# Performance work log

Measured on AMD Instinct MI355X. Metric: run time of the kernel, lower is better.

The kernel has to match this reference:

```python
import jax, jax.numpy as jnp
import numpy as np

N = 50000      # nodes
E = 800000     # edges in normalized A (incl. self loops)
DIN = 128      # input_dim
DOUT = 64      # output_dim
BN_EPS = 1e-5
SLOPE = 0.01   # LeakyReLU default negative slope


def setup_inputs() -> dict:
    key = jax.random.key(0)
    ks = jax.random.split(key, 10)
    H = jax.random.normal(ks[0], (N, DIN), dtype=jnp.float32)
    rows = jax.random.randint(ks[1], (E,), 0, N, dtype=jnp.int32)
    cols = jax.random.randint(ks[2], (E,), 0, N, dtype=jnp.int32)
    # values of the symmetrically normalized adjacency (precomputed in __init__)
    vals = jax.random.uniform(ks[3], (E,), dtype=jnp.float32)
    # BatchNorm1d params/buffers (eval mode: use running stats)
    gamma = 1.0 + 0.1 * jax.random.normal(ks[4], (DIN,), dtype=jnp.float32)
    beta = 0.1 * jax.random.normal(ks[5], (DIN,), dtype=jnp.float32)
    run_mean = 0.1 * jax.random.normal(ks[6], (DIN,), dtype=jnp.float32)
    run_var = 0.5 + jax.random.uniform(ks[7], (DIN,), dtype=jnp.float32)
    # Linear(input_dim, output_dim)
    W = jax.random.normal(ks[8], (DIN, DOUT), dtype=jnp.float32) / np.sqrt(DIN)
    b = 0.01 * jax.random.normal(ks[9], (DOUT,), dtype=jnp.float32)
    return dict(H=H, rows=rows, cols=cols, vals=vals, gamma=gamma, beta=beta,
                run_mean=run_mean, run_var=run_var, W=W, b=b)


def reference(H, rows, cols, vals, gamma, beta, run_mean, run_var, W, b):
    # F.normalize: L2 row normalization with eps=1e-12
    norm = jnp.maximum(jnp.linalg.norm(H, axis=1, keepdims=True), 1e-12)
    Hn = H / norm
    # BatchNorm1d (eval: running stats); dropout is identity in eval
    scale = gamma * jax.lax.rsqrt(run_var + BN_EPS)
    Hb = (Hn - run_mean) * scale + beta
    # Linear projection [N, DIN] @ [DIN, DOUT]
    X = Hb @ W + b
    # SpMM: out[r] = sum_{e: rows[e]==r} vals[e] * X[cols[e]]
    msgs = vals[:, None] * X[cols]            # [E, DOUT] gather + scale
    out = jax.ops.segment_sum(msgs, rows, num_segments=N)
    # LeakyReLU
    return jnp.where(out >= 0, out, SLOPE * out)
```

## Files before the change

kernel.cpp:

```cpp
#include <hip/hip_runtime.h>

#define N_NODES 50000
#define E_EDGES 800000
#define DIN 128
#define DOUT 64
#define NBUK 196
#define CHUNK 4096
#define NBLKA 196
#define ASTRIDE 136

typedef short short8 __attribute__((ext_vector_type(8)));
typedef float f32x4 __attribute__((ext_vector_type(4)));

static __device__ __forceinline__ short f2bf(float f)
{
    union { float f; unsigned u; } x{f};
    const unsigned r = x.u + 0x7FFFu + ((x.u >> 16) & 1u);
    return (short)(r >> 16);
}

__global__ void k_prep(const float* __restrict__ W, const float* __restrict__ gamma,
                       const float* __restrict__ beta, const float* __restrict__ mean,
                       const float* __restrict__ var,
                       unsigned short* __restrict__ Wt, float* __restrict__ sc,
                       float* __restrict__ sh)
{
    const int idx = blockIdx.x * 256 + threadIdx.x;
    const int n = idx >> 7, k = idx & 127;
    Wt[n * DIN + k] = (unsigned short)f2bf(W[k * DOUT + n]);
    if (idx < DIN) {
        const float s = gamma[idx] / sqrtf(var[idx] + 1e-5f);
        sc[idx] = s;
        sh[idx] = beta[idx] - mean[idx] * s;
    }
}

__global__ __launch_bounds__(256) void k_x(
    const float* __restrict__ H, const float* __restrict__ sc,
    const float* __restrict__ sh, const unsigned short* __restrict__ Wt,
    const float* __restrict__ bias, float* __restrict__ X)
{
    __shared__ short A_s[64][ASTRIDE];
    __shared__ short B_s[64][ASTRIDE];
    const int t = threadIdx.x;
    const int l = t & 63, wv = t >> 6;
    const int R0 = blockIdx.x * 64;

    {
        const int rloc = t >> 2, sub = t & 3;
        const int r = R0 + rloc;
        float4 h[8];
        if (r < N_NODES) {
            const float4* hp = (const float4*)(H + (size_t)r * DIN + sub * 32);
#pragma unroll
            for (int i = 0; i < 8; ++i) h[i] = hp[i];
        } else {
#pragma unroll
            for (int i = 0; i < 8; ++i) h[i] = make_float4(0.f, 0.f, 0.f, 0.f);
        }
        float ss = 0.f;
#pragma unroll
        for (int i = 0; i < 8; ++i)
            ss += h[i].x * h[i].x + h[i].y * h[i].y + h[i].z * h[i].z + h[i].w * h[i].w;
        ss += __shfl_xor(ss, 1, 64);
        ss += __shfl_xor(ss, 2, 64);
        const float inv = 1.0f / fmaxf(sqrtf(ss), 1e-12f);

        const float4* scp = (const float4*)(sc + sub * 32);
        const float4* shp = (const float4*)(sh + sub * 32);
#pragma unroll
        for (int i = 0; i < 8; ++i) {
            const float4 s4 = scp[i], b4 = shp[i];
            const float e0 = h[i].x * inv * s4.x + b4.x;
            const float e1 = h[i].y * inv * s4.y + b4.y;
            const float e2 = h[i].z * inv * s4.z + b4.z;
            const float e3 = h[i].w * inv * s4.w + b4.w;
            const unsigned u0 = (unsigned short)f2bf(e0) | ((unsigned)(unsigned short)f2bf(e1) << 16);
            const unsigned u1 = (unsigned short)f2bf(e2) | ((unsigned)(unsigned short)f2bf(e3) << 16);
            *(uint2*)&A_s[rloc][sub * 32 + i * 4] = make_uint2(u0, u1);
        }
    }
    {
        const int n = t >> 2, koff = (t & 3) * 32;
        const uint4* src = (const uint4*)(Wt + n * DIN + koff);
#pragma unroll
        for (int i = 0; i < 4; ++i)
            *(uint4*)&B_s[n][koff + i * 8] = src[i];
    }
    __syncthreads();

    const int ml = l & 15, q = l >> 4;
    f32x4 c0, c1, c2, c3;
    {
        const float b0 = bias[ml],      b1 = bias[16 + ml];
        const float b2 = bias[32 + ml], b3 = bias[48 + ml];
        c0 = f32x4{b0, b0, b0, b0};
        c1 = f32x4{b1, b1, b1, b1};
        c2 = f32x4{b2, b2, b2, b2};
        c3 = f32x4{b3, b3, b3, b3};
    }
#pragma unroll
    for (int k0 = 0; k0 < 4; ++k0) {
        const short8 a  = *(const short8*)&A_s[wv * 16 + ml][k0 * 32 + q * 8];
        const short8 b0 = *(const short8*)&B_s[ml][k0 * 32 + q * 8];
        const short8 b1 = *(const short8*)&B_s[16 + ml][k0 * 32 + q * 8];
        const short8 b2 = *(const short8*)&B_s[32 + ml][k0 * 32 + q * 8];
        const short8 b3 = *(const short8*)&B_s[48 + ml][k0 * 32 + q * 8];
        c0 = __builtin_amdgcn_mfma_f32_16x16x32_bf16(a, b0, c0, 0, 0, 0);
        c1 = __builtin_amdgcn_mfma_f32_16x16x32_bf16(a, b1, c1, 0, 0, 0);
        c2 = __builtin_amdgcn_mfma_f32_16x16x32_bf16(a, b2, c2, 0, 0, 0);
        c3 = __builtin_amdgcn_mfma_f32_16x16x32_bf16(a, b3, c3, 0, 0, 0);
    }
#pragma unroll
    for (int i = 0; i < 4; ++i) {
        const int row = R0 + wv * 16 + q * 4 + i;
        if (row < N_NODES) {
            float* xr = X + (size_t)row * DOUT;
            xr[ml]      = c0[i];
            xr[16 + ml] = c1[i];
            xr[32 + ml] = c2[i];
            xr[48 + ml] = c3[i];
        }
    }
}

__global__ __launch_bounds__(1024) void k_bhist(
    const int* __restrict__ rows, int* __restrict__ hist)
{
    __shared__ int lh[NBUK];
    const int t = threadIdx.x;
    if (t < NBUK) lh[t] = 0;
    __syncthreads();
    const int e0 = blockIdx.x * 8192;
#pragma unroll
    for (int k = 0; k < 8; ++k) {
        const int e = e0 + k * 1024 + t;
        if (e < E_EDGES) atomicAdd(&lh[rows[e] >> 8], 1);
    }
    __syncthreads();
    if (t < NBUK) {
        const int c = lh[t];
        if (c) atomicAdd(&hist[t], c);
    }
}

__global__ __launch_bounds__(256) void k_bscan(
    const int* __restrict__ hist, int* __restrict__ gstart, int* __restrict__ gcursor)
{
    __shared__ int scn[256];
    const int t = threadIdx.x;
    const int v = (t < NBUK) ? hist[t] : 0;
    scn[t] = v;
    __syncthreads();
    for (int o = 1; o < 256; o <<= 1) {
        const int u = (t >= o) ? scn[t - o] : 0;
        __syncthreads();
        scn[t] += u;
        __syncthreads();
    }
    const int ex = scn[t] - v;
    if (t < NBUK) { gstart[t] = ex; gcursor[t] = ex; }
    if (t == NBUK - 1) gstart[NBUK] = ex + v;
}

__global__ __launch_bounds__(256) void k_passA(
    const int* __restrict__ rows, const int* __restrict__ cols,
    const float* __restrict__ vals, int* __restrict__ gcursor,
    uint2* __restrict__ mid)
{
    __shared__ int lhist[NBUK], lstart[NBUK], lcur[NBUK], gbase[NBUK];
    __shared__ int scn[256];
    __shared__ uint2 lbin[CHUNK];
    const int t = threadIdx.x;
    const int e0 = blockIdx.x * CHUNK;
    const int nC = min(CHUNK, E_EDGES - e0);

    if (t < NBUK) lhist[t] = 0;
    __syncthreads();

    uint2 pr[16];
#pragma unroll
    for (int k = 0; k < 16; ++k) {
        const int e = e0 + k * 256 + t;
        if (e < E_EDGES) {
            const int r = rows[e];
            const unsigned pk = (unsigned)cols[e] | ((unsigned)(r & 255) << 16)
                              | ((unsigned)(r >> 8) << 24);
            pr[k] = make_uint2(__float_as_uint(vals[e]), pk);
            atomicAdd(&lhist[r >> 8], 1);
        } else {
            pr[k] = make_uint2(0u, 0xFFFFFFFFu);
        }
    }
    __syncthreads();

    const int v = (t < NBUK) ? lhist[t] : 0;
    scn[t] = v;
    __syncthreads();
    for (int o = 1; o < 256; o <<= 1) {
        const int u = (t >= o) ? scn[t - o] : 0;
        __syncthreads();
        scn[t] += u;
        __syncthreads();
    }
    if (t < NBUK) {
        const int ex = scn[t] - v;
        lstart[t] = ex;
        lcur[t] = ex;
        gbase[t] = v ? atomicAdd(&gcursor[t], v) : 0;
    }
    __syncthreads();

#pragma unroll
    for (int k = 0; k < 16; ++k) {
        const unsigned pk = pr[k].y;
        if (pk != 0xFFFFFFFFu) {
            const int b = pk >> 24;
            const int pos = atomicAdd(&lcur[b], 1);
            lbin[pos] = pr[k];
        }
    }
    __syncthreads();

    for (int i = t; i < nC; i += 256) {
        const uint2 p = lbin[i];
        const int b = p.y >> 24;
        mid[gbase[b] + (i - lstart[b])] = p;
    }
}

__global__ __launch_bounds__(256) void k_passB(
    const int* __restrict__ gstart, const uint2* __restrict__ mid,
    uint2* __restrict__ ev, int* __restrict__ startRow)
{
    __shared__ int lhist[256], scn[256], lcur[256];
    const int t = threadIdx.x;
    const int b = blockIdx.x;
    const int s = gstart[b], e2 = gstart[b + 1];

    lhist[t] = 0;
    __syncthreads();
    for (int i = s + t; i < e2; i += 256)
        atomicAdd(&lhist[(mid[i].y >> 16) & 255], 1);
    __syncthreads();

    const int v = lhist[t];
    scn[t] = v;
    __syncthreads();
    for (int o = 1; o < 256; o <<= 1) {
        const int u = (t >= o) ? scn[t - o] : 0;
        __syncthreads();
        scn[t] += u;
        __syncthreads();
    }
    const int ex = scn[t] - v;
    lcur[t] = ex;
    const int gr = b * 256 + t;
    if (gr <= N_NODES) startRow[gr] = s + ex;
    __syncthreads();

    for (int i = s + t; i < e2; i += 256) {
        const uint2 p = mid[i];
        const int r8 = (p.y >> 16) & 255;
        const int pos = atomicAdd(&lcur[r8], 1);
        ev[s + pos] = make_uint2(p.x, p.y & 0xFFFFu);
    }
}

__global__ __launch_bounds__(256) void k_spmm(
    const int* __restrict__ start, const uint2* __restrict__ ev,
    const float* __restrict__ X, float* __restrict__ out)
{
    const int lane = threadIdx.x & 63;
    const int row  = blockIdx.x * 4 + (threadIdx.x >> 6);
    if (row >= N_NODES) return;
    const int s  = __builtin_amdgcn_readfirstlane(start[row]);
    const int e2 = __builtin_amdgcn_readfirstlane(start[row + 1]);
    float acc = 0.f;
    int c = s;
    for (; c + 3 < e2; c += 4) {
        const uint2 p0 = ev[c],     p1 = ev[c + 1];
        const uint2 p2 = ev[c + 2], p3 = ev[c + 3];
        const float x0 = X[(int)p0.y * DOUT + lane];
        const float x1 = X[(int)p1.y * DOUT + lane];
        const float x2 = X[(int)p2.y * DOUT + lane];
        const float x3 = X[(int)p3.y * DOUT + lane];
        acc = fmaf(__uint_as_float(p0.x), x0, acc);
        acc = fmaf(__uint_as_float(p1.x), x1, acc);
        acc = fmaf(__uint_as_float(p2.x), x2, acc);
        acc = fmaf(__uint_as_float(p3.x), x3, acc);
    }
    for (; c < e2; ++c) {
        const uint2 p = ev[c];
        acc = fmaf(__uint_as_float(p.x), X[(int)p.y * DOUT + lane], acc);
    }
    out[(size_t)row * DOUT + lane] = (acc >= 0.f) ? acc : 0.01f * acc;
}

extern "C" void kernel_launch(void* const* d_in, const int* in_sizes, int n_in,
                              void* d_out, int out_size, void* d_ws, size_t ws_size,
                              hipStream_t stream)
{
    const float* H     = (const float*)d_in[0];
    const int*   rows  = (const int*)  d_in[1];
    const int*   cols  = (const int*)  d_in[2];
    const float* vals  = (const float*)d_in[3];
    const float* gamma = (const float*)d_in[4];
    const float* beta  = (const float*)d_in[5];
    const float* mean  = (const float*)d_in[6];
    const float* var   = (const float*)d_in[7];
    const float* W     = (const float*)d_in[8];
    const float* bias  = (const float*)d_in[9];
    float* out = (float*)d_out;

    char* ws = (char*)d_ws;
    float*          X        = (float*)(ws);
    int*            hist     = (int*)  (ws + 12800000);
    int*            gstart   = (int*)  (ws + 12800800);
    int*            gcursor  = (int*)  (ws + 12801600);
    int*            startRow = (int*)  (ws + 12802400);
    uint2*          mid      = (uint2*)(ws + 13002416);
    uint2*          ev       = (uint2*)(ws + 19402416);
    unsigned short* Wt       = (unsigned short*)(ws + 25802416);
    float*          sc       = (float*)(ws + 25818800);
    float*          sh       = (float*)(ws + 25819312);

    hipMemsetAsync(hist, 0, NBUK * sizeof(int), stream);

    k_prep<<<32, 256, 0, stream>>>(W, gamma, beta, mean, var, Wt, sc, sh);
    k_x<<<(N_NODES + 63) / 64, 256, 0, stream>>>(H, sc, sh, Wt, bias, X);
    k_bhist<<<(E_EDGES + 8191) / 8192, 1024, 0, stream>>>(rows, hist);
    k_bscan<<<1, 256, 0, stream>>>(hist, gstart, gcursor);
    k_passA<<<NBLKA, 256, 0, stream>>>(rows, cols, vals, gcursor, mid);
    k_passB<<<NBUK, 256, 0, stream>>>(gstart, mid, ev, startRow);
    k_spmm<<<(N_NODES + 3) / 4, 256, 0, stream>>>(startRow, ev, X, out);
}
```

Before: 166.9 us.

## Restructure CSR build with fixed-capacity buckets, per-row counts, and half-wave SpMM

Drops the separate bucket-histogram and bucket-scan kernels. Pass A now writes into fixed-capacity bucket regions and counts edges per row with global atomics. A two-level row scan plus an atomic scatter pass replaces the per-bucket sort in pass B, and the SpMM now handles two rows per wave. Each lane loads a float2, and edge metadata is broadcast with shuffles. The intent is fewer launches, more parallel blocks and wider gathers, at the cost of about 800k global atomics, non-deterministic edge order within a row, and a risk of overflow if any bucket exceeds BUKCAP.

```diff
diff --git a/kernel.cpp b/kernel.cpp
--- a/kernel.cpp
+++ b/kernel.cpp
@@ -5,8 +5,7 @@
 #define DIN 128
 #define DOUT 64
 #define NBUK 196
-#define CHUNK 4096
-#define NBLKA 196
+#define BUKCAP 4608
 #define ASTRIDE 136
 
 typedef short short8 __attribute__((ext_vector_type(8)));
@@ -124,32 +123,39 @@
     }
 }
 
-__global__ __launch_bounds__(1024) void k_bhist(
-    const int* __restrict__ rows, int* __restrict__ hist)
-{
-    __shared__ int lh[NBUK];
+__global__ __launch_bounds__(256) void k_passA(
+    const int* __restrict__ rows, const int* __restrict__ cols,
+    const float* __restrict__ vals, int* __restrict__ cnt,
+    int* __restrict__ gcursor, uint2* __restrict__ mid)
+{
+    __shared__ int lhist[NBUK], lstart[NBUK], lcur[NBUK], gbase[NBUK];
+    __shared__ int scn[256];
+    __shared__ uint2 lbin[1024];
     const int t = threadIdx.x;
-    if (t < NBUK) lh[t] = 0;
-    __syncthreads();
-    const int e0 = blockIdx.x * 8192;
-#pragma unroll
-    for (int k = 0; k < 8; ++k) {
-        const int e = e0 + k * 1024 + t;
-        if (e < E_EDGES) atomicAdd(&lh[rows[e] >> 8], 1);
-    }
-    __syncthreads();
-    if (t < NBUK) {
-        const int c = lh[t];
-        if (c) atomicAdd(&hist[t], c);
-    }
-}
-
-__global__ __launch_bounds__(256) void k_bscan(
-    const int* __restrict__ hist, int* __restrict__ gstart, int* __restrict__ gcursor)
-{
-    __shared__ int scn[256];
-    const int t = threadIdx.x;
-    const int v = (t < NBUK) ? hist[t] : 0;
+    const int e0 = blockIdx.x * 1024;
+    const int nC = min(1024, E_EDGES - e0);
+
+    if (t < NBUK) lhist[t] = 0;
+    __syncthreads();
+
+    uint2 pr[4];
+#pragma unroll
+    for (int k = 0; k < 4; ++k) {
+        const int e = e0 + k * 256 + t;
+        if (e < E_EDGES) {
+            const int r = rows[e];
+            pr[k] = make_uint2(__float_as_uint(vals[e]),
+                               (unsigned)cols[e] | ((unsigned)(r & 255) << 16)
+                                                 | ((unsigned)(r >> 8) << 24));
+            atomicAdd(&lhist[r >> 8], 1);
+            atomicAdd(&cnt[r], 1);
+        } else {
+            pr[k] = make_uint2(0u, 0xFFFFFFFFu);
+        }
+    }
+    __syncthreads();
+
+    const int v = (t < NBUK) ? lhist[t] : 0;
     scn[t] = v;
     __syncthreads();
     for (int o = 1; o < 256; o <<= 1) {
@@ -158,143 +164,156 @@
         scn[t] += u;
         __syncthreads();
     }
-    const int ex = scn[t] - v;
-    if (t < NBUK) { gstart[t] = ex; gcursor[t] = ex; }
-    if (t == NBUK - 1) gstart[NBUK] = ex + v;
-}
-
-__global__ __launch_bounds__(256) void k_passA(
-    const int* __restrict__ rows, const int* __restrict__ cols,
-    const float* __restrict__ vals, int* __restrict__ gcursor,
-    uint2* __restrict__ mid)
-{
-    __shared__ int lhist[NBUK], lstart[NBUK], lcur[NBUK], gbase[NBUK];
-    __shared__ int scn[256];
-    __shared__ uint2 lbin[CHUNK];
-    const int t = threadIdx.x;
-    const int e0 = blockIdx.x * CHUNK;
-    const int nC = min(CHUNK, E_EDGES - e0);
-
-    if (t < NBUK) lhist[t] = 0;
-    __syncthreads();
-
-    uint2 pr[16];
-#pragma unroll
-    for (int k = 0; k < 16; ++k) {
-        const int e = e0 + k * 256 + t;
-        if (e < E_EDGES) {
-            const int r = rows[e];
-            const unsigned pk = (unsigned)cols[e] | ((unsigned)(r & 255) << 16)
-                              | ((unsigned)(r >> 8) << 24);
-            pr[k] = make_uint2(__float_as_uint(vals[e]), pk);
-            atomicAdd(&lhist[r >> 8], 1);
-        } else {
-            pr[k] = make_uint2(0u, 0xFFFFFFFFu);
-        }
-    }
-    __syncthreads();
-
-    const int v = (t < NBUK) ? lhist[t] : 0;
-    scn[t] = v;
-    __syncthreads();
-    for (int o = 1; o < 256; o <<= 1) {
-        const int u = (t >= o) ? scn[t - o] : 0;
-        __syncthreads();
-        scn[t] += u;
-        __syncthreads();
-    }
     if (t < NBUK) {
         const int ex = scn[t] - v;
         lstart[t] = ex;
         lcur[t] = ex;
-        gbase[t] = v ? atomicAdd(&gcursor[t], v) : 0;
-    }
-    __syncthreads();
-
-#pragma unroll
-    for (int k = 0; k < 16; ++k) {
+        gbase[t] = t * BUKCAP + (v ? atomicAdd(&gcursor[t], v) : 0);
+    }
+    __syncthreads();
+
+#pragma unroll
+    for (int k = 0; k < 4; ++k) {
         const unsigned pk = pr[k].y;
         if (pk != 0xFFFFFFFFu) {
-            const int b = pk >> 24;
-            const int pos = atomicAdd(&lcur[b], 1);
-            lbin[pos] = pr[k];
+            const int bk = pk >> 24;
+            lbin[atomicAdd(&lcur[bk], 1)] = pr[k];
         }
     }
     __syncthreads();
 
     for (int i = t; i < nC; i += 256) {
         const uint2 p = lbin[i];
-        const int b = p.y >> 24;
-        mid[gbase[b] + (i - lstart[b])] = p;
-    }
-}
-
-__global__ __launch_bounds__(256) void k_passB(
-    const int* __restrict__ gstart, const uint2* __restrict__ mid,
-    uint2* __restrict__ ev, int* __restrict__ startRow)
-{
-    __shared__ int lhist[256], scn[256], lcur[256];
-    const int t = threadIdx.x;
-    const int b = blockIdx.x;
-    const int s = gstart[b], e2 = gstart[b + 1];
-
-    lhist[t] = 0;
-    __syncthreads();
-    for (int i = s + t; i < e2; i += 256)
-        atomicAdd(&lhist[(mid[i].y >> 16) & 255], 1);
-    __syncthreads();
-
-    const int v = lhist[t];
-    scn[t] = v;
-    __syncthreads();
-    for (int o = 1; o < 256; o <<= 1) {
-        const int u = (t >= o) ? scn[t - o] : 0;
-        __syncthreads();
-        scn[t] += u;
-        __syncthreads();
-    }
-    const int ex = scn[t] - v;
-    lcur[t] = ex;
-    const int gr = b * 256 + t;
-    if (gr <= N_NODES) startRow[gr] = s + ex;
-    __syncthreads();
-
-    for (int i = s + t; i < e2; i += 256) {
-        const uint2 p = mid[i];
-        const int r8 = (p.y >> 16) & 255;
-        const int pos = atomicAdd(&lcur[r8], 1);
-        ev[s + pos] = make_uint2(p.x, p.y & 0xFFFFu);
+        const int bk = p.y >> 24;
+        mid[gbase[bk] + (i - lstart[bk])] = p;
+    }
+}
+
+__global__ __launch_bounds__(256) void k_rscan1(
+    const int* __restrict__ cnt, int* __restrict__ startL,
+    int* __restrict__ cursorL, int* __restrict__ bsum)
+{
+    const int b = blockIdx.x, t = threadIdx.x;
+    const int base = b * 1024 + t * 4;
+    int c0 = 0, c1 = 0, c2 = 0, c3 = 0;
+    if (base + 3 < N_NODES) {
+        const int4 c = *(const int4*)(cnt + base);
+        c0 = c.x; c1 = c.y; c2 = c.z; c3 = c.w;
+    } else {
+        if (base     < N_NODES) c0 = cnt[base];
+        if (base + 1 < N_NODES) c1 = cnt[base + 1];
+        if (base + 2 < N_NODES) c2 = cnt[base + 2];
+        if (base + 3 < N_NODES) c3 = cnt[base + 3];
+    }
+    const int s = c0 + c1 + c2 + c3;
+    const int lane = t & 63, wv = t >> 6;
+    int x = s;
+#pragma unroll
+    for (int o = 1; o < 64; o <<= 1) {
+        const int y = __shfl_up(x, o, 64);
+        if (lane >= o) x += y;
+    }
+    __shared__ int wsum[4];
+    if (lane == 63) wsum[wv] = x;
+    __syncthreads();
+    int wpre = 0;
+    for (int i = 0; i < wv; ++i) wpre += wsum[i];
+    const int ex = wpre + x - s;
+    const int p0 = ex, p1 = ex + c0, p2 = p1 + c1, p3 = p2 + c2;
+    if (base + 3 < N_NODES) {
+        *(int4*)(startL + base)  = make_int4(p0, p1, p2, p3);
+        *(int4*)(cursorL + base) = make_int4(p0, p1, p2, p3);
+    } else {
+        const int pv[4] = {p0, p1, p2, p3};
+        for (int i = 0; i < 4; ++i) {
+            if (base + i <= N_NODES) startL[base + i] = pv[i];
+            if (base + i <  N_NODES) cursorL[base + i] = pv[i];
+        }
+    }
+    if (t == 255) bsum[b] = ex + s;
+}
+
+__global__ void k_rscan2(const int* __restrict__ bsum, int* __restrict__ boff)
+{
+    const int lane = threadIdx.x;
+    const int v = (lane < 49) ? bsum[lane] : 0;
+    int x = v;
+#pragma unroll
+    for (int o = 1; o < 64; o <<= 1) {
+        const int y = __shfl_up(x, o, 64);
+        if (lane >= o) x += y;
+    }
+    if (lane < 49) boff[lane] = x - v;
+}
+
+__global__ __launch_bounds__(256) void k_scatter2(
+    const int* __restrict__ gcursor, const uint2* __restrict__ mid,
+    int* __restrict__ cursorL, const int* __restrict__ boff,
+    uint2* __restrict__ ev)
+{
+    const int b  = blockIdx.x / 5;
+    const int sl = blockIdx.x % 5;
+    const int cntb = gcursor[b];
+    const int i0 = sl * 1024;
+    if (i0 >= cntb) return;
+    const int i1 = min(i0 + 1024, cntb);
+    const uint2* src = mid + (size_t)b * BUKCAP;
+    for (int i = i0 + threadIdx.x; i < i1; i += 256) {
+        const uint2 p = src[i];
+        const int row = (b << 8) | ((int)(p.y >> 16) & 255);
+        const int pos = atomicAdd(&cursorL[row], 1) + boff[row >> 10];
+        ev[pos] = make_uint2(p.x, p.y & 0xFFFFu);
     }
 }
 
 __global__ __launch_bounds__(256) void k_spmm(
-    const int* __restrict__ start, const uint2* __restrict__ ev,
-    const float* __restrict__ X, float* __restrict__ out)
+    const int* __restrict__ startL, const int* __restrict__ boff,
+    const uint2* __restrict__ ev, const float* __restrict__ X,
+    float* __restrict__ out)
 {
     const int lane = threadIdx.x & 63;
-    const int row  = blockIdx.x * 4 + (threadIdx.x >> 6);
-    if (row >= N_NODES) return;
-    const int s  = __builtin_amdgcn_readfirstlane(start[row]);
-    const int e2 = __builtin_amdgcn_readfirstlane(start[row + 1]);
-    float acc = 0.f;
-    int c = s;
-    for (; c + 3 < e2; c += 4) {
-        const uint2 p0 = ev[c],     p1 = ev[c + 1];
-        const uint2 p2 = ev[c + 2], p3 = ev[c + 3];
-        const float x0 = X[(int)p0.y * DOUT + lane];
-        const float x1 = X[(int)p1.y * DOUT + lane];
-        const float x2 = X[(int)p2.y * DOUT + lane];
-        const float x3 = X[(int)p3.y * DOUT + lane];
-        acc = fmaf(__uint_as_float(p0.x), x0, acc);
-        acc = fmaf(__uint_as_float(p1.x), x1, acc);
-        acc = fmaf(__uint_as_float(p2.x), x2, acc);
-        acc = fmaf(__uint_as_float(p3.x), x3, acc);
-    }
-    for (; c < e2; ++c) {
-        const uint2 p = ev[c];
-        acc = fmaf(__uint_as_float(p.x), X[(int)p.y * DOUT + lane], acc);
-    }
-    out[(size_t)row * DOUT + lane] = (acc >= 0.f) ? acc : 0.01f * acc;
+    const int hl   = lane & 31;
+    const int sb   = lane & 32;
+    const int row  = blockIdx.x * 8 + ((threadIdx.x >> 6) << 1) + (lane >> 5);
+    const int s  = startL[row] + boff[row >> 10];
+    const int e2 = startL[row + 1] + boff[(row + 1) >> 10];
+    float2 acc = make_float2(0.f, 0.f);
+    for (int c = s; c < e2; c += 32) {
+        const int idx = c + hl;
+        uint2 p = make_uint2(0u, 0u);
+        if (idx < e2) p = ev[idx];
+        const int cnt = min(e2 - c, 32);
+        int j = 0;
+        for (; j + 3 < cnt; j += 4) {
+            const float v0 = __uint_as_float(__shfl((int)p.x, sb + j,     64));
+            const int   c0 = __shfl((int)p.y, sb + j,     64) & 0xFFFF;
+            const float v1 = __uint_as_float(__shfl((int)p.x, sb + j + 1, 64));
+            const int   c1 = __shfl((int)p.y, sb + j + 1, 64) & 0xFFFF;
+            const float v2 = __uint_as_float(__shfl((int)p.x, sb + j + 2, 64));
+            const int   c2 = __shfl((int)p.y, sb + j + 2, 64) & 0xFFFF;
+            const float v3 = __uint_as_float(__shfl((int)p.x, sb + j + 3, 64));
+            const int   c3 = __shfl((int)p.y, sb + j + 3, 64) & 0xFFFF;
+            const float2 x0 = *(const float2*)(X + c0 * DOUT + hl * 2);
+            const float2 x1 = *(const float2*)(X + c1 * DOUT + hl * 2);
+            const float2 x2 = *(const float2*)(X + c2 * DOUT + hl * 2);
+            const float2 x3 = *(const float2*)(X + c3 * DOUT + hl * 2);
+            acc.x = fmaf(v0, x0.x, acc.x); acc.y = fmaf(v0, x0.y, acc.y);
+            acc.x = fmaf(v1, x1.x, acc.x); acc.y = fmaf(v1, x1.y, acc.y);
+            acc.x = fmaf(v2, x2.x, acc.x); acc.y = fmaf(v2, x2.y, acc.y);
+            acc.x = fmaf(v3, x3.x, acc.x); acc.y = fmaf(v3, x3.y, acc.y);
+        }
+        for (; j < cnt; ++j) {
+            const float v = __uint_as_float(__shfl((int)p.x, sb + j, 64));
+            const int  cc = __shfl((int)p.y, sb + j, 64) & 0xFFFF;
+            const float2 xx = *(const float2*)(X + cc * DOUT + hl * 2);
+            acc.x = fmaf(v, xx.x, acc.x);
+            acc.y = fmaf(v, xx.y, acc.y);
+        }
+    }
+    float2 r;
+    r.x = (acc.x >= 0.f) ? acc.x : 0.01f * acc.x;
+    r.y = (acc.y >= 0.f) ? acc.y : 0.01f * acc.y;
+    *(float2*)(out + (size_t)row * DOUT + hl * 2) = r;
 }
 
 extern "C" void kernel_launch(void* const* d_in, const int* in_sizes, int n_in,
@@ -314,24 +333,26 @@
     float* out = (float*)d_out;
 
     char* ws = (char*)d_ws;
-    float*          X        = (float*)(ws);
-    int*            hist     = (int*)  (ws + 12800000);
-    int*            gstart   = (int*)  (ws + 12800800);
-    int*            gcursor  = (int*)  (ws + 12801600);
-    int*            startRow = (int*)  (ws + 12802400);
-    uint2*          mid      = (uint2*)(ws + 13002416);
-    uint2*          ev       = (uint2*)(ws + 19402416);
-    unsigned short* Wt       = (unsigned short*)(ws + 25802416);
-    float*          sc       = (float*)(ws + 25818800);
-    float*          sh       = (float*)(ws + 25819312);
-
-    hipMemsetAsync(hist, 0, NBUK * sizeof(int), stream);
+    float*          X       = (float*)(ws);
+    int*            cnt     = (int*)  (ws + 12800000);
+    int*            gcursor = (int*)  (ws + 13000000);
+    int*            startL  = (int*)  (ws + 13000800);
+    int*            cursorL = (int*)  (ws + 13200816);
+    int*            bsum    = (int*)  (ws + 13400816);
+    int*            boff    = (int*)  (ws + 13401024);
+    uint2*          mid     = (uint2*)(ws + 13401280);
+    uint2*          ev      = (uint2*)(ws + 20626624);
+    unsigned short* Wt      = (unsigned short*)(ws + 27026624);
+    float*          sc      = (float*)(ws + 27043008);
+    float*          sh      = (float*)(ws + 27043520);
+
+    hipMemsetAsync(cnt, 0, 200784, stream);
 
     k_prep<<<32, 256, 0, stream>>>(W, gamma, beta, mean, var, Wt, sc, sh);
     k_x<<<(N_NODES + 63) / 64, 256, 0, stream>>>(H, sc, sh, Wt, bias, X);
-    k_bhist<<<(E_EDGES + 8191) / 8192, 1024, 0, stream>>>(rows, hist);
-    k_bscan<<<1, 256, 0, stream>>>(hist, gstart, gcursor);
-    k_passA<<<NBLKA, 256, 0, stream>>>(rows, cols, vals, gcursor, mid);
-    k_passB<<<NBUK, 256, 0, stream>>>(gstart, mid, ev, startRow);
-    k_spmm<<<(N_NODES + 3) / 4, 256, 0, stream>>>(startRow, ev, X, out);
-}
+    k_passA<<<(E_EDGES + 1023) / 1024, 256, 0, stream>>>(rows, cols, vals, cnt, gcursor, mid);
+    k_rscan1<<<49, 256, 0, stream>>>(cnt, startL, cursorL, bsum);
+    k_rscan2<<<1, 64, 0, stream>>>(bsum, boff);
+    k_scatter2<<<NBUK * 5, 256, 0, stream>>>(gcursor, mid, cursorL, boff, ev);
+    k_spmm<<<N_NODES / 8, 256, 0, stream>>>(startL, boff, ev, X, out);
+}
```

After: 208.1 us. 24.7% more time.

## Replace two-pass CSR build with fixed-capacity row buckets and LDS-atomic SpMM

Applied to the files above, without the earlier changes.

Drops the global bucket histogram, the scan and the second sort pass. Pass A now scatters packed edges straight into fixed-capacity slots per 256-row bucket. The new SpMM gives each bucket one 1024-thread block, which accumulates results with float atomics into 64 KB of LDS and applies LeakyReLU on write-out. This removes kernel launches and a full read/write pass over the edges. The costs are LDS atomic contention, only 196 large blocks, and silent edge loss if any bucket exceeds the fixed capacity, which is only safe for near-uniform row distributions.

```diff
diff --git a/kernel.cpp b/kernel.cpp
--- a/kernel.cpp
+++ b/kernel.cpp
@@ -5,8 +5,9 @@
 #define DIN 128
 #define DOUT 64
 #define NBUK 196
-#define CHUNK 4096
-#define NBLKA 196
+#define BUKCAP 4608
+#define CHUNK 2048
+#define NBLKA 391
 #define ASTRIDE 136
 
 typedef short short8 __attribute__((ext_vector_type(8)));
@@ -124,45 +125,6 @@
     }
 }
 
-__global__ __launch_bounds__(1024) void k_bhist(
-    const int* __restrict__ rows, int* __restrict__ hist)
-{
-    __shared__ int lh[NBUK];
-    const int t = threadIdx.x;
-    if (t < NBUK) lh[t] = 0;
-    __syncthreads();
-    const int e0 = blockIdx.x * 8192;
-#pragma unroll
-    for (int k = 0; k < 8; ++k) {
-        const int e = e0 + k * 1024 + t;
-        if (e < E_EDGES) atomicAdd(&lh[rows[e] >> 8], 1);
-    }
-    __syncthreads();
-    if (t < NBUK) {
-        const int c = lh[t];
-        if (c) atomicAdd(&hist[t], c);
-    }
-}
-
-__global__ __launch_bounds__(256) void k_bscan(
-    const int* __restrict__ hist, int* __restrict__ gstart, int* __restrict__ gcursor)
-{
-    __shared__ int scn[256];
-    const int t = threadIdx.x;
-    const int v = (t < NBUK) ? hist[t] : 0;
-    scn[t] = v;
-    __syncthreads();
-    for (int o = 1; o < 256; o <<= 1) {
-        const int u = (t >= o) ? scn[t - o] : 0;
-        __syncthreads();
-        scn[t] += u;
-        __syncthreads();
-    }
-    const int ex = scn[t] - v;
-    if (t < NBUK) { gstart[t] = ex; gcursor[t] = ex; }
-    if (t == NBUK - 1) gstart[NBUK] = ex + v;
-}
-
 __global__ __launch_bounds__(256) void k_passA(
     const int* __restrict__ rows, const int* __restrict__ cols,
     const float* __restrict__ vals, int* __restrict__ gcursor,
@@ -178,15 +140,15 @@
     if (t < NBUK) lhist[t] = 0;
     __syncthreads();
 
-    uint2 pr[16];
-#pragma unroll
-    for (int k = 0; k < 16; ++k) {
+    uint2 pr[8];
+#pragma unroll
+    for (int k = 0; k < 8; ++k) {
         const int e = e0 + k * 256 + t;
         if (e < E_EDGES) {
             const int r = rows[e];
-            const unsigned pk = (unsigned)cols[e] | ((unsigned)(r & 255) << 16)
-                              | ((unsigned)(r >> 8) << 24);
-            pr[k] = make_uint2(__float_as_uint(vals[e]), pk);
+            pr[k] = make_uint2(__float_as_uint(vals[e]),
+                               (unsigned)cols[e] | ((unsigned)(r & 255) << 16)
+                                                 | ((unsigned)(r >> 8) << 24));
             atomicAdd(&lhist[r >> 8], 1);
         } else {
             pr[k] = make_uint2(0u, 0xFFFFFFFFu);
@@ -207,94 +169,84 @@
         const int ex = scn[t] - v;
         lstart[t] = ex;
         lcur[t] = ex;
-        gbase[t] = v ? atomicAdd(&gcursor[t], v) : 0;
-    }
-    __syncthreads();
-
-#pragma unroll
-    for (int k = 0; k < 16; ++k) {
+        gbase[t] = t * BUKCAP + (v ? atomicAdd(&gcursor[t], v) : 0);
+    }
+    __syncthreads();
+
+#pragma unroll
+    for (int k = 0; k < 8; ++k) {
         const unsigned pk = pr[k].y;
         if (pk != 0xFFFFFFFFu) {
-            const int b = pk >> 24;
-            const int pos = atomicAdd(&lcur[b], 1);
-            lbin[pos] = pr[k];
+            const int bk = pk >> 24;
+            lbin[atomicAdd(&lcur[bk], 1)] = pr[k];
         }
     }
     __syncthreads();
 
     for (int i = t; i < nC; i += 256) {
         const uint2 p = lbin[i];
-        const int b = p.y >> 24;
-        mid[gbase[b] + (i - lstart[b])] = p;
-    }
-}
-
-__global__ __launch_bounds__(256) void k_passB(
-    const int* __restrict__ gstart, const uint2* __restrict__ mid,
-    uint2* __restrict__ ev, int* __restrict__ startRow)
-{
-    __shared__ int lhist[256], scn[256], lcur[256];
+        const int bk = p.y >> 24;
+        const int idx = gbase[bk] + (i - lstart[bk]);
+        if (idx < (bk + 1) * BUKCAP)
+            mid[idx] = p;
+    }
+}
+
+__global__ __launch_bounds__(1024) void k_spmm2(
+    const int* __restrict__ gcursor, const uint2* __restrict__ mid,
+    const float* __restrict__ X, float* __restrict__ out)
+{
+    __shared__ float acc[256 * DOUT];
     const int t = threadIdx.x;
     const int b = blockIdx.x;
-    const int s = gstart[b], e2 = gstart[b + 1];
-
-    lhist[t] = 0;
-    __syncthreads();
-    for (int i = s + t; i < e2; i += 256)
-        atomicAdd(&lhist[(mid[i].y >> 16) & 255], 1);
-    __syncthreads();
-
-    const int v = lhist[t];
-    scn[t] = v;
-    __syncthreads();
-    for (int o = 1; o < 256; o <<= 1) {
-        const int u = (t >= o) ? scn[t - o] : 0;
-        __syncthreads();
-        scn[t] += u;
-        __syncthreads();
-    }
-    const int ex = scn[t] - v;
-    lcur[t] = ex;
-    const int gr = b * 256 + t;
-    if (gr <= N_NODES) startRow[gr] = s + ex;
-    __syncthreads();
-
-    for (int i = s + t; i < e2; i += 256) {
-        const uint2 p = mid[i];
-        const int r8 = (p.y >> 16) & 255;
-        const int pos = atomicAdd(&lcur[r8], 1);
-        ev[s + pos] = make_uint2(p.x, p.y & 0xFFFFu);
-    }
-}
-
-__global__ __launch_bounds__(256) void k_spmm(
-    const int* __restrict__ start, const uint2* __restrict__ ev,
-    const float* __restrict__ X, float* __restrict__ out)
-{
-    const int lane = threadIdx.x & 63;
-    const int row  = blockIdx.x * 4 + (threadIdx.x >> 6);
-    if (row >= N_NODES) return;
-    const int s  = __builtin_amdgcn_readfirstlane(start[row]);
-    const int e2 = __builtin_amdgcn_readfirstlane(start[row + 1]);
-    float acc = 0.f;
-    int c = s;
-    for (; c + 3 < e2; c += 4) {
-        const uint2 p0 = ev[c],     p1 = ev[c + 1];
-        const uint2 p2 = ev[c + 2], p3 = ev[c + 3];
-        const float x0 = X[(int)p0.y * DOUT + lane];
-        const float x1 = X[(int)p1.y * DOUT + lane];
-        const float x2 = X[(int)p2.y * DOUT + lane];
-        const float x3 = X[(int)p3.y * DOUT + lane];
-        acc = fmaf(__uint_as_float(p0.x), x0, acc);
-        acc = fmaf(__uint_as_float(p1.x), x1, acc);
-        acc = fmaf(__uint_as_float(p2.x), x2, acc);
-        acc = fmaf(__uint_as_float(p3.x), x3, acc);
-    }
-    for (; c < e2; ++c) {
-        const uint2 p = ev[c];
-        acc = fmaf(__uint_as_float(p.x), X[(int)p.y * DOUT + lane], acc);
-    }
-    out[(size_t)row * DOUT + lane] = (acc >= 0.f) ? acc : 0.01f * acc;
+    const int lane = t & 63;
+
+    float4* accv = (float4*)acc;
+#pragma unroll
+    for (int k = 0; k < 4; ++k)
+        accv[k * 1024 + t] = make_float4(0.f, 0.f, 0.f, 0.f);
+    __syncthreads();
+
+    const int total = min(__builtin_amdgcn_readfirstlane(gcursor[b]), BUKCAP);
+    const int wv = __builtin_amdgcn_readfirstlane(threadIdx.x >> 6);
+    const int L  = (total + 15) >> 4;
+    const int cs = wv * L;
+    const int ce = min(cs + L, total);
+    const uint2* src = mid + (size_t)b * BUKCAP;
+
+    int c = cs;
+    for (; c + 3 < ce; c += 4) {
+        const uint2 p0 = src[c],     p1 = src[c + 1];
+        const uint2 p2 = src[c + 2], p3 = src[c + 3];
+        const float x0 = X[(int)(p0.y & 0xFFFFu) * DOUT + lane];
+        const float x1 = X[(int)(p1.y & 0xFFFFu) * DOUT + lane];
+        const float x2 = X[(int)(p2.y & 0xFFFFu) * DOUT + lane];
+        const float x3 = X[(int)(p3.y & 0xFFFFu) * DOUT + lane];
+        atomicAdd(&acc[(int)((p0.y >> 16) & 255u) * DOUT + lane], __uint_as_float(p0.x) * x0);
+        atomicAdd(&acc[(int)((p1.y >> 16) & 255u) * DOUT + lane], __uint_as_float(p1.x) * x1);
+        atomicAdd(&acc[(int)((p2.y >> 16) & 255u) * DOUT + lane], __uint_as_float(p2.x) * x2);
+        atomicAdd(&acc[(int)((p3.y >> 16) & 255u) * DOUT + lane], __uint_as_float(p3.x) * x3);
+    }
+    for (; c < ce; ++c) {
+        const uint2 p = src[c];
+        const float x = X[(int)(p.y & 0xFFFFu) * DOUT + lane];
+        atomicAdd(&acc[(int)((p.y >> 16) & 255u) * DOUT + lane], __uint_as_float(p.x) * x);
+    }
+    __syncthreads();
+
+    const int r0 = b << 8;
+#pragma unroll
+    for (int k = 0; k < 4; ++k) {
+        const int off = k * 4096 + t * 4;
+        if (r0 + (off >> 6) < N_NODES) {
+            float4 a = *(float4*)&acc[off];
+            a.x = (a.x >= 0.f) ? a.x : 0.01f * a.x;
+            a.y = (a.y >= 0.f) ? a.y : 0.01f * a.y;
+            a.z = (a.z >= 0.f) ? a.z : 0.01f * a.z;
+            a.w = (a.w >= 0.f) ? a.w : 0.01f * a.w;
+            *(float4*)(out + (size_t)r0 * DOUT + off) = a;
+        }
+    }
 }
 
 extern "C" void kernel_launch(void* const* d_in, const int* in_sizes, int n_in,
@@ -314,24 +266,17 @@
     float* out = (float*)d_out;
 
     char* ws = (char*)d_ws;
-    float*          X        = (float*)(ws);
-    int*            hist     = (int*)  (ws + 12800000);
-    int*            gstart   = (int*)  (ws + 12800800);
-    int*            gcursor  = (int*)  (ws + 12801600);
-    int*            startRow = (int*)  (ws + 12802400);
-    uint2*          mid      = (uint2*)(ws + 13002416);
-    uint2*          ev       = (uint2*)(ws + 19402416);
-    unsigned short* Wt       = (unsigned short*)(ws + 25802416);
-    float*          sc       = (float*)(ws + 25818800);
-    float*          sh       = (float*)(ws + 25819312);
-
-    hipMemsetAsync(hist, 0, NBUK * sizeof(int), stream);
+    float*          X       = (float*)(ws);
+    int*            gcursor = (int*)  (ws + 12800000);
+    uint2*          mid     = (uint2*)(ws + 12800800);
+    unsigned short* Wt      = (unsigned short*)(ws + 20026144);
+    float*          sc      = (float*)(ws + 20042528);
+    float*          sh      = (float*)(ws + 20043040);
+
+    hipMemsetAsync(gcursor, 0, NBUK * sizeof(int), stream);
 
     k_prep<<<32, 256, 0, stream>>>(W, gamma, beta, mean, var, Wt, sc, sh);
     k_x<<<(N_NODES + 63) / 64, 256, 0, stream>>>(H, sc, sh, Wt, bias, X);
-    k_bhist<<<(E_EDGES + 8191) / 8192, 1024, 0, stream>>>(rows, hist);
-    k_bscan<<<1, 256, 0, stream>>>(hist, gstart, gcursor);
     k_passA<<<NBLKA, 256, 0, stream>>>(rows, cols, vals, gcursor, mid);
-    k_passB<<<NBUK, 256, 0, stream>>>(gstart, mid, ev, startRow);
-    k_spmm<<<(N_NODES + 3) / 4, 256, 0, stream>>>(startRow, ev, X, out);
-}
+    k_spmm2<<<NBUK, 1024, 0, stream>>>(gcursor, mid, X, out);
+}
```

Measured after the change: 468.2 us. 181% more time.
